# Kernel tuning notes

Measured on AMD Instinct MI355X. Metric: run time of the kernel, lower is better.

## Reference

```python
import jax, jax.numpy as jnp
import numpy as np

NMS_THR = 0.3


def pairwise_iou(b):
    # b: [N,4] in x1,y1,x2,y2
    area = (b[:, 2] - b[:, 0]) * (b[:, 3] - b[:, 1])  # [N]
    x1 = jnp.maximum(b[:, None, 0], b[None, :, 0])
    y1 = jnp.maximum(b[:, None, 1], b[None, :, 1])
    x2 = jnp.minimum(b[:, None, 2], b[None, :, 2])
    y2 = jnp.minimum(b[:, None, 3], b[None, :, 3])
    inter = jnp.clip(x2 - x1, 0.0) * jnp.clip(y2 - y1, 0.0)
    return inter / (area[:, None] + area[None, :] - inter + 1e-9)


def nms_keep(boxes, scores, valid, thr):
    # greedy NMS, fixed-shape: returns bool keep mask in original order
    N = boxes.shape[0]
    order = jnp.argsort(-jnp.where(valid, scores, -jnp.inf))
    b = boxes[order]
    v = valid[order]
    iou = pairwise_iou(b)  # [N,N]

    def step(keep, i):
        suppressed = jnp.any(keep & (iou[i] > thr))
        keep = keep.at[i].set(v[i] & jnp.logical_not(suppressed))
        return keep, None

    keep_sorted, _ = jax.lax.scan(step, jnp.zeros((N,), dtype=bool), jnp.arange(N))
    return jnp.zeros((N,), dtype=bool).at[order].set(keep_sorted)


def setup_inputs() -> dict:
    key = jax.random.key(0)
    k1, k2, k3, k4 = jax.random.split(key, 4)
    N, C, S = 6000, 81, 800
    # well-formed proposals: x1,y1 in [0, 600), w,h in [8, 200)
    xy = jax.random.uniform(k1, (N, 2), dtype=jnp.float32) * 600.0
    wh = 8.0 + jax.random.uniform(k2, (N, 2), dtype=jnp.float32) * 192.0
    proposals = jnp.concatenate([xy, xy + wh], axis=1)  # [N,4]
    reg = jax.random.normal(k3, (N, C * 4), dtype=jnp.float32)
    clss = jax.random.normal(k4, (N, C), dtype=jnp.float32) * 2.0
    stds = jnp.array([0.1, 0.1, 0.2, 0.2], dtype=jnp.float32)
    return {"proposals": proposals, "reg": reg, "clss": clss, "stds": stds, "img_size": S}


def reference(proposals, reg, clss, stds, img_size):
    N, C = clss.shape
    # anchors_bbox2offset: x1y1x2y2 -> center x,y + w,h
    w = proposals[:, 2] - proposals[:, 0]
    h = proposals[:, 3] - proposals[:, 1]
    cx = proposals[:, 0] + 0.5 * w
    cy = proposals[:, 1] + 0.5 * h
    # class selection
    probs = jax.nn.softmax(clss, axis=1)
    cls_idx = jnp.argmax(probs, axis=1)  # [N]
    score = jnp.take_along_axis(probs, cls_idx[:, None], axis=1)[:, 0]
    valid = cls_idx != 0  # non-background
    reg4 = reg.reshape(N, C, 4)
    t = jnp.take_along_axis(reg4, cls_idx[:, None, None], axis=1)[:, 0, :] * stds  # [N,4]
    # decode
    px = cx + w * t[:, 0]
    py = cy + h * t[:, 1]
    pw = w * jnp.exp(t[:, 2])
    ph = h * jnp.exp(t[:, 3])
    # offset2bbox + clip
    hi = jnp.float32(img_size - 1)
    x1 = jnp.clip(px - 0.5 * pw, 0.0, hi)
    y1 = jnp.clip(py - 0.5 * ph, 0.0, hi)
    x2 = jnp.clip(px + 0.5 * pw, 0.0, hi)
    y2 = jnp.clip(py + 0.5 * ph, 0.0, hi)
    boxes = jnp.stack((x1, y1, x2, y2), axis=1)  # [N,4]
    keep = nms_keep(jax.lax.stop_gradient(boxes), jax.lax.stop_gradient(score), valid, NMS_THR)
    m = keep.astype(boxes.dtype)
    return boxes * m[:, None], score * m, cls_idx * keep.astype(cls_idx.dtype)
```

## Files before the change

### kernel.cpp

```cpp
#include <hip/hip_runtime.h>
#include <math.h>

#define NMS_THR 0.3f
#define NACC 8

__device__ __forceinline__ float fmul(float a, float b){ return __fmul_rn(a,b); }
__device__ __forceinline__ float fadd(float a, float b){ return __fadd_rn(a,b); }
__device__ __forceinline__ float fsub(float a, float b){ return __fsub_rn(a,b); }

#define BAR_LDS() asm volatile("s_waitcnt lgkmcnt(0)\n\ts_barrier" ::: "memory")

__device__ __forceinline__ unsigned long long rdlane64(unsigned long long v, int a) {
    unsigned long long l = (unsigned int)__builtin_amdgcn_readlane((int)(unsigned int)v, a);
    unsigned long long h = (unsigned int)__builtin_amdgcn_readlane((int)(unsigned int)(v >> 32), a);
    return (h << 32) | l;
}
__device__ __forceinline__ unsigned long long rfl64(unsigned long long x){
    unsigned int lo = (unsigned int)__builtin_amdgcn_readfirstlane((int)(unsigned int)x);
    unsigned int hi = (unsigned int)__builtin_amdgcn_readfirstlane((int)(unsigned int)(x >> 32));
    return ((unsigned long long)hi << 32) | lo;
}
__device__ __forceinline__ unsigned long long waveOr64(unsigned long long v){
    for (int o = 32; o > 0; o >>= 1) v |= __shfl_xor(v, o);
    return v;
}

__global__ __launch_bounds__(256) void k_decode(
    const float* __restrict__ prop, const float* __restrict__ reg,
    const float* __restrict__ clss, const float* __restrict__ stds,
    const int* __restrict__ imgsz,
    float* __restrict__ boxes, float* __restrict__ key,
    float* __restrict__ score, int* __restrict__ cls,
    int N, int C)
{
    int wid  = threadIdx.x >> 6;
    int lane = threadIdx.x & 63;
    int n = blockIdx.x * 4 + wid;
    if (n >= N) return;
    const float* row = clss + (long)n * C;
    float ninf = -__builtin_inff();
    float x0 = (lane < C)      ? row[lane]      : ninf;
    float x1 = (lane + 64 < C) ? row[lane + 64] : ninf;
    float m = fmaxf(x0, x1);
    for (int o = 32; o > 0; o >>= 1) m = fmaxf(m, __shfl_xor(m, o));
    float e0 = (lane < C)      ? expf(x0 - m) : 0.0f;
    float e1 = (lane + 64 < C) ? expf(x1 - m) : 0.0f;
    float s = e0 + e1;
    for (int o = 32; o > 0; o >>= 1) s += __shfl_xor(s, o);
    float bv; int bi;
    if (e0 >= e1) { bv = e0; bi = lane; } else { bv = e1; bi = lane + 64; }
    for (int o = 32; o > 0; o >>= 1) {
        float ov = __shfl_xor(bv, o);
        int   oi = __shfl_xor(bi, o);
        if (ov > bv || (ov == bv && oi < bi)) { bv = ov; bi = oi; }
    }
    if (lane == 0) {
        float sc = 1.0f / s;
        int   c  = bi;
        int   valid = (c != 0);
        float p0 = prop[n*4+0], p1 = prop[n*4+1], p2 = prop[n*4+2], p3 = prop[n*4+3];
        float w  = fsub(p2, p0), h = fsub(p3, p1);
        float cx = fadd(p0, fmul(0.5f, w));
        float cy = fadd(p1, fmul(0.5f, h));
        const float* rr = reg + (long)n * C * 4 + (long)c * 4;
        float t0 = fmul(rr[0], stds[0]);
        float t1 = fmul(rr[1], stds[1]);
        float t2 = fmul(rr[2], stds[2]);
        float t3 = fmul(rr[3], stds[3]);
        float px = fadd(cx, fmul(w, t0));
        float py = fadd(cy, fmul(h, t1));
        float pw = fmul(w, expf(t2));
        float ph = fmul(h, expf(t3));
        float hi = (float)(imgsz[0] - 1);
        float bx1 = fminf(fmaxf(fsub(px, fmul(0.5f, pw)), 0.0f), hi);
        float by1 = fminf(fmaxf(fsub(py, fmul(0.5f, ph)), 0.0f), hi);
        float bx2 = fminf(fmaxf(fadd(px, fmul(0.5f, pw)), 0.0f), hi);
        float by2 = fminf(fmaxf(fadd(py, fmul(0.5f, ph)), 0.0f), hi);
        boxes[n*4+0]=bx1; boxes[n*4+1]=by1; boxes[n*4+2]=bx2; boxes[n*4+3]=by2;
        score[n] = sc;
        cls[n]   = c;
        key[n]   = valid ? sc : ninf;
    }
}

__global__ __launch_bounds__(256) void k_rank(
    const float* __restrict__ key, const float* __restrict__ boxes,
    float* __restrict__ boxesSorted, float* __restrict__ areaSorted,
    float* __restrict__ keySorted, int* __restrict__ rank,
    int* __restrict__ nValidPtr, int N)
{
    extern __shared__ float lkey[];
    __shared__ int part[256];
    int tid = threadIdx.x;
    for (int j = tid; j < N; j += 256) lkey[j] = key[j];
    __syncthreads();

    int i = blockIdx.x * 64 + (tid & 63);
    int s = tid >> 6;
    int Q = (N + 3) >> 2;
    int r_part = 0;
    if (i < N) {
        float ki = lkey[i];
        int j0 = s * Q, j1 = min(N, j0 + Q);
        for (int j = j0; j < j1; ++j) {
            float kj = lkey[j];
            r_part += (kj > ki) || (kj == ki && j < i);
        }
    }
    part[tid] = r_part;
    __syncthreads();

    if (tid < 64 && i < N) {
        int r = part[tid] + part[tid+64] + part[tid+128] + part[tid+192];
        float ki = lkey[i];
        rank[i] = r;
        float b0 = boxes[i*4+0], b1 = boxes[i*4+1], b2 = boxes[i*4+2], b3 = boxes[i*4+3];
        boxesSorted[r*4+0]=b0; boxesSorted[r*4+1]=b1; boxesSorted[r*4+2]=b2; boxesSorted[r*4+3]=b3;
        areaSorted[r] = fmul(fsub(b2,b0), fsub(b3,b1));
        keySorted[r]  = ki;
    }

    if (blockIdx.x == 0) {
        __syncthreads();
        float ninf = -__builtin_inff();
        int inv = 0;
        for (int j = tid; j < N; j += 256) inv += (lkey[j] == ninf);
        part[tid] = inv;
        __syncthreads();
        if (tid == 0) {
            int t = 0;
            for (int q = 0; q < 256; ++q) t += part[q];
            nValidPtr[0] = N - t;
        }
    }
}

__global__ __launch_bounds__(256) void k_mask(
    const float* __restrict__ bs, const float* __restrict__ areas,
    const float* __restrict__ keySorted, unsigned long long* __restrict__ mask,
    unsigned long long* __restrict__ dq,
    int N, int W, int Wpad)
{
    int wid  = threadIdx.x >> 6;
    int lane = threadIdx.x & 63;
    int i = blockIdx.x * 4 + wid;
    if (i >= N) return;
    if (keySorted[i] == -__builtin_inff()) return;
    float ax1 = bs[i*4+0], ay1 = bs[i*4+1], ax2 = bs[i*4+2], ay2 = bs[i*4+3];
    float aa  = areas[i];
    int w0 = i >> 6;
    if (lane == 0) {
        dq[i*4+0] = 0ULL; dq[i*4+1] = 0ULL; dq[i*4+2] = 0ULL; dq[i*4+3] = 0ULL;
    }
    for (int w = w0; w < W; ++w) {
        int j = w*64 + lane;
        int bit = 0;
        if (j < N && j > i) {
            float bx1 = bs[j*4+0], by1 = bs[j*4+1], bx2 = bs[j*4+2], by2 = bs[j*4+3];
            float ba  = areas[j];
            float ix1 = fmaxf(ax1,bx1), iy1 = fmaxf(ay1,by1);
            float ix2 = fminf(ax2,bx2), iy2 = fminf(ay2,by2);
            float iw = fmaxf(fsub(ix2,ix1), 0.0f);
            float ih = fmaxf(fsub(iy2,iy1), 0.0f);
            float inter = fmul(iw, ih);
            float denom = fadd(fsub(fadd(aa, ba), inter), 1e-9f);
            float iou = inter / denom;
            bit = (iou > NMS_THR) ? 1 : 0;
        }
        unsigned long long bm = __ballot(bit);
        if (lane == 0) {
            mask[(long)i*Wpad + w] = bm;
            int d = w - w0;
            if (d < 4) dq[i*4+d] = bm;
        }
    }
}

__global__ __launch_bounds__((NACC+1)*64, 1) void k_scan(
    const unsigned long long* __restrict__ mask,
    const unsigned long long* __restrict__ dq,
    const int* __restrict__ nValidPtr,
    int* __restrict__ keepSorted, int N, int W, int Wpad)
{
    __shared__ unsigned long long ldsPartA[NACC+1];
    __shared__ unsigned long long ldsPartB[NACC+1];
    __shared__ unsigned long long ldsKeepLo, ldsKeepHi;
    int tid  = threadIdx.x;
    int wid  = tid >> 6;
    int lane = tid & 63;
    for (int i = tid; i < N; i += (NACC+1)*64) keepSorted[i] = 0;
    if (tid <= NACC) { ldsPartA[tid] = 0ULL; ldsPartB[tid] = 0ULL; }
    if (tid == 0) { ldsKeepLo = 0ULL; ldsKeepHi = 0ULL; }
    __syncthreads();

    int nValid  = __builtin_amdgcn_readfirstlane(nValidPtr[0]);
    int nChunks = (nValid + 127) >> 7;

    unsigned long long A0=0,A1=0,A2=0,A3=0,B0=0,B1=0,B2=0,B3=0;
    unsigned long long sacc_prevA = 0ULL, sacc_prevB = 0ULL;
    if (wid == 0 && nChunks > 0) {
        int rA = lane, rB = 64 + lane;
        if (rA < N) {
            ulonglong2 a01 = *(const ulonglong2*)(dq + (size_t)rA*4);
            ulonglong2 a23 = *(const ulonglong2*)(dq + (size_t)rA*4 + 2);
            A0=a01.x; A1=a01.y; A2=a23.x; A3=a23.y;
        }
        if (rB < N) {
            ulonglong2 b01 = *(const ulonglong2*)(dq + (size_t)rB*4);
            ulonglong2 b23 = *(const ulonglong2*)(dq + (size_t)rB*4 + 2);
            B0=b01.x; B1=b01.y; B2=b23.x; B3=b23.y;
        }
    }
    unsigned long long accx = 0ULL, accy = 0ULL;
    bool accWave = (wid >= 1);
    int  accIdx  = wid - 1;
    bool laneok  = (2*lane + 1 < Wpad);

    for (int c = 0; c < nChunks; ++c) {
        int base = c << 7;
        if (wid == 0) {
            unsigned long long nA0=0,nA1=0,nA2=0,nA3=0,nB0=0,nB1=0,nB2=0,nB3=0;
            if (c + 1 < nChunks) {
                int rA = base + 128 + lane, rB = base + 192 + lane;
                if (rA < N) {
                    ulonglong2 a01 = *(const ulonglong2*)(dq + (size_t)rA*4);
                    ulonglong2 a23 = *(const ulonglong2*)(dq + (size_t)rA*4 + 2);
                    nA0=a01.x; nA1=a01.y; nA2=a23.x; nA3=a23.y;
                }
                if (rB < N) {
                    ulonglong2 b01 = *(const ulonglong2*)(dq + (size_t)rB*4);
                    ulonglong2 b23 = *(const ulonglong2*)(dq + (size_t)rB*4 + 2);
                    nB0=b01.x; nB1=b01.y; nB2=b23.x; nB3=b23.y;
                }
            }

            unsigned long long pA = sacc_prevA, pB = sacc_prevB;
#pragma unroll
            for (int k = 1; k <= NACC; ++k) { pA |= ldsPartA[k]; pB |= ldsPartB[k]; }
            unsigned long long incLo = rfl64(pA), incHi = rfl64(pB);
            int nv  = nValid - base;
            unsigned long long validLo = (nv >= 64) ? ~0ULL : ((1ULL << nv) - 1ULL);
            int nv2 = nv - 64;
            unsigned long long validHi = (nv2 >= 64) ? ~0ULL
                                        : (nv2 <= 0 ? 0ULL : ((1ULL << nv2) - 1ULL));
            unsigned long long candLo = validLo & ~incLo;
            unsigned long long candHi = validHi & ~incHi;
            unsigned long long keepLo = 0ULL, keepHi = 0ULL;

            unsigned long long mHiAcc = 0ULL;
            while (candLo) {
                unsigned long long t = candLo;
                int a0 = __builtin_ctzll(t); t &= t - 1;
                int a1 = t ? __builtin_ctzll(t) : a0; t &= t - 1;
                int a2 = t ? __builtin_ctzll(t) : a0; t &= t - 1;
                int a3 = t ? __builtin_ctzll(t) : a0;
                unsigned long long m0 = rdlane64(A0, a0), m1 = rdlane64(A0, a1);
                unsigned long long m2 = rdlane64(A0, a2), m3 = rdlane64(A0, a3);
                unsigned long long n0 = rdlane64(A1, a0), n1 = rdlane64(A1, a1);
                unsigned long long n2 = rdlane64(A1, a2), n3 = rdlane64(A1, a3);
                unsigned long long rem  = m0 | (1ULL << a0);
                unsigned long long kept = 1ULL << a0;
                unsigned long long hi   = n0;
                unsigned long long b;
                b = 1ULL << a1; if (!(rem & b)) { rem |= m1 | b; kept |= b; hi |= n1; }
                b = 1ULL << a2; if (!(rem & b)) { rem |= m2 | b; kept |= b; hi |= n2; }
                b = 1ULL << a3; if (!(rem & b)) { rem |= m3 | b; kept |= b; hi |= n3; }
                keepLo |= kept; mHiAcc |= hi;
                candLo &= ~rem;
            }
            candHi &= ~mHiAcc;
            while (candHi) {
                unsigned long long t = candHi;
                int a0 = __builtin_ctzll(t); t &= t - 1;
                int a1 = t ? __builtin_ctzll(t) : a0; t &= t - 1;
                int a2 = t ? __builtin_ctzll(t) : a0; t &= t - 1;
                int a3 = t ? __builtin_ctzll(t) : a0;
                unsigned long long m0 = rdlane64(B0, a0), m1 = rdlane64(B0, a1);
                unsigned long long m2 = rdlane64(B0, a2), m3 = rdlane64(B0, a3);
                unsigned long long rem  = m0 | (1ULL << a0);
                unsigned long long kept = 1ULL << a0;
                unsigned long long b;
                b = 1ULL << a1; if (!(rem & b)) { rem |= m1 | b; kept |= b; }
                b = 1ULL << a2; if (!(rem & b)) { rem |= m2 | b; kept |= b; }
                b = 1ULL << a3; if (!(rem & b)) { rem |= m3 | b; kept |= b; }
                keepHi |= kept;
                candHi &= ~rem;
            }
            {
                unsigned long long kL = (keepLo >> lane) & 1ULL;
                unsigned long long kH = (keepHi >> lane) & 1ULL;
                unsigned long long selA = (kL ? A2 : 0ULL) | (kH ? B1 : 0ULL);
                unsigned long long selB = (kL ? A3 : 0ULL) | (kH ? B2 : 0ULL);
                sacc_prevA = waveOr64(selA);
                sacc_prevB = waveOr64(selB);
            }
            if (lane == 0) { ldsKeepLo = keepLo; ldsKeepHi = keepHi; }
            if (base + lane < N)      keepSorted[base + lane]      = (int)((keepLo >> lane) & 1ULL);
            if (base + 64 + lane < N) keepSorted[base + 64 + lane] = (int)((keepHi >> lane) & 1ULL);
            A0=nA0; A1=nA1; A2=nA2; A3=nA3; B0=nB0; B1=nB1; B2=nB2; B3=nB3;
        }
        BAR_LDS();
        unsigned long long kLo = ldsKeepLo;
        unsigned long long kHi = ldsKeepHi;
        if (accWave && laneok && lane == c + 1) {
            ldsPartA[wid] = accx;
            ldsPartB[wid] = accy;
        }
        BAR_LDS();
        if (accWave && laneok) {
            unsigned int myb = (accIdx < 4)
                ? (unsigned int)((kLo >> (16*accIdx)) & 0xFFFFULL)
                : (unsigned int)((kHi >> (16*(accIdx-4))) & 0xFFFFULL);
            if (myb) {
                const unsigned long long* mb =
                    mask + (size_t)(base + 16*accIdx) * Wpad + 2*lane;
                unsigned int b = myb;
                int a0 = __builtin_ctz(b); b &= b - 1;
                int a1=-1,a2=-1,a3=-1,a4=-1,a5=-1,a6=-1,a7=-1;
                if (b) { a1 = __builtin_ctz(b); b &= b - 1; }
                if (b) { a2 = __builtin_ctz(b); b &= b - 1; }
                if (b) { a3 = __builtin_ctz(b); b &= b - 1; }
                if (b) { a4 = __builtin_ctz(b); b &= b - 1; }
                if (b) { a5 = __builtin_ctz(b); b &= b - 1; }
                if (b) { a6 = __builtin_ctz(b); b &= b - 1; }
                if (b) { a7 = __builtin_ctz(b); b &= b - 1; }
                ulonglong2 v0 = {0,0}, v1 = {0,0}, v2 = {0,0}, v3 = {0,0};
                ulonglong2 v4 = {0,0}, v5 = {0,0}, v6 = {0,0}, v7 = {0,0};
                v0 = *(const ulonglong2*)(mb + (size_t)a0 * Wpad);
                if (a1 >= 0) v1 = *(const ulonglong2*)(mb + (size_t)a1 * Wpad);
                if (a2 >= 0) v2 = *(const ulonglong2*)(mb + (size_t)a2 * Wpad);
                if (a3 >= 0) v3 = *(const ulonglong2*)(mb + (size_t)a3 * Wpad);
                if (a4 >= 0) v4 = *(const ulonglong2*)(mb + (size_t)a4 * Wpad);
                if (a5 >= 0) v5 = *(const ulonglong2*)(mb + (size_t)a5 * Wpad);
                if (a6 >= 0) v6 = *(const ulonglong2*)(mb + (size_t)a6 * Wpad);
                if (a7 >= 0) v7 = *(const ulonglong2*)(mb + (size_t)a7 * Wpad);
                accx |= ((v0.x|v1.x)|(v2.x|v3.x)) | ((v4.x|v5.x)|(v6.x|v7.x));
                accy |= ((v0.y|v1.y)|(v2.y|v3.y)) | ((v4.y|v5.y)|(v6.y|v7.y));
                while (b) {
                    int a = __builtin_ctz(b); b &= b - 1;
                    ulonglong2 v = *(const ulonglong2*)(mb + (size_t)a * Wpad);
                    accx |= v.x; accy |= v.y;
                }
            }
        }
    }
}

__global__ __launch_bounds__(256) void k_out(
    const float* __restrict__ boxes, const float* __restrict__ score,
    const int* __restrict__ cls, const int* __restrict__ rank,
    const int* __restrict__ keepSorted,
    float* __restrict__ out, int N)
{
    int n = blockIdx.x * blockDim.x + threadIdx.x;
    if (n >= N) return;
    int k = keepSorted[rank[n]];
    float m = (float)k;
    out[n*4+0] = boxes[n*4+0]*m;
    out[n*4+1] = boxes[n*4+1]*m;
    out[n*4+2] = boxes[n*4+2]*m;
    out[n*4+3] = boxes[n*4+3]*m;
    out[(long)N*4 + n] = score[n]*m;
    out[(long)N*5 + n] = (float)(cls[n] * k);
}

extern "C" void kernel_launch(void* const* d_in, const int* in_sizes, int n_in,
                              void* d_out, int out_size, void* d_ws, size_t ws_size,
                              hipStream_t stream) {
    const float* prop = (const float*)d_in[0];
    const float* reg  = (const float*)d_in[1];
    const float* clss = (const float*)d_in[2];
    const float* stds = (const float*)d_in[3];
    const int*   img  = (const int*)d_in[4];

    int N = in_sizes[0] / 4;
    int C = in_sizes[2] / N;
    int W = (N + 63) / 64;
    int Wpad = (W + 1) & ~1;

    char* ws = (char*)d_ws;
    size_t off = 0;
    float* boxes       = (float*)(ws + off); off += (size_t)N*4*sizeof(float);
    float* key         = (float*)(ws + off); off += (size_t)N*sizeof(float);
    float* score       = (float*)(ws + off); off += (size_t)N*sizeof(float);
    int*   cls         = (int*)  (ws + off); off += (size_t)N*sizeof(int);
    int*   rank        = (int*)  (ws + off); off += (size_t)N*sizeof(int);
    float* boxesSorted = (float*)(ws + off); off += (size_t)N*4*sizeof(float);
    float* areaSorted  = (float*)(ws + off); off += (size_t)N*sizeof(float);
    float* keySorted   = (float*)(ws + off); off += (size_t)N*sizeof(float);
    int*   keepSorted  = (int*)  (ws + off); off += (size_t)N*sizeof(int);
    int*   nValid      = (int*)  (ws + off); off += sizeof(int);
    off = (off + 31) & ~(size_t)31;
    unsigned long long* dq    = (unsigned long long*)(ws + off);
    off += (size_t)N * 4 * sizeof(unsigned long long);
    unsigned long long* mask  = (unsigned long long*)(ws + off);
    off += (size_t)N * Wpad * sizeof(unsigned long long);
    (void)ws_size; (void)out_size; (void)n_in;

    int rowBlocks  = (N + 3) / 4;
    int thrBlocks  = (N + 255) / 256;
    int rankBlocks = (N + 63) / 64;

    k_decode<<<rowBlocks, 256, 0, stream>>>(prop, reg, clss, stds, img,
                                            boxes, key, score, cls, N, C);
    k_rank<<<rankBlocks, 256, (size_t)N*sizeof(float), stream>>>(key, boxes,
                                            boxesSorted, areaSorted, keySorted, rank, nValid, N);
    k_mask<<<rowBlocks, 256, 0, stream>>>(boxesSorted, areaSorted, keySorted,
                                          mask, dq, N, W, Wpad);
    k_scan<<<1, (NACC+1)*64, 0, stream>>>(mask, dq, nValid, keepSorted, N, W, Wpad);
    k_out<<<thrBlocks, 256, 0, stream>>>(boxes, score, cls, rank, keepSorted,
                                         (float*)d_out, N);
}
```

Before: 185.9 us.

## Use backward-suppression bitmasks and ballot for serial in-chunk NMS resolution

The mask kernel now also emits per-row backward masks: bdiag holds the in-word earlier boxes that overlap each box, and bprev holds the overlaps against the preceding word for odd words. In the scan kernel, the sequential greedy loop within each 64-box word becomes a single ballot over the lanes' backward masks per kept box. This replaces the four-at-a-time readlane gathering of forward masks, cutting the serial dependency chain and the register traffic per step. The cost is extra IoU work and two additional small arrays written in the mask kernel, plus more ballot instructions in the loop.

Result: faster. 181.0 us (-2.7%).

```diff
diff --git a/kernel.cpp b/kernel.cpp
--- a/kernel.cpp
+++ b/kernel.cpp
@@ -10,11 +10,6 @@
 
 #define BAR_LDS() asm volatile("s_waitcnt lgkmcnt(0)\n\ts_barrier" ::: "memory")
 
-__device__ __forceinline__ unsigned long long rdlane64(unsigned long long v, int a) {
-    unsigned long long l = (unsigned int)__builtin_amdgcn_readlane((int)(unsigned int)v, a);
-    unsigned long long h = (unsigned int)__builtin_amdgcn_readlane((int)(unsigned int)(v >> 32), a);
-    return (h << 32) | l;
-}
 __device__ __forceinline__ unsigned long long rfl64(unsigned long long x){
     unsigned int lo = (unsigned int)__builtin_amdgcn_readfirstlane((int)(unsigned int)x);
     unsigned int hi = (unsigned int)__builtin_amdgcn_readfirstlane((int)(unsigned int)(x >> 32));
@@ -139,6 +134,7 @@
     const float* __restrict__ bs, const float* __restrict__ areas,
     const float* __restrict__ keySorted, unsigned long long* __restrict__ mask,
     unsigned long long* __restrict__ dq,
+    unsigned long long* __restrict__ bdiag, unsigned long long* __restrict__ bprev,
     int N, int W, int Wpad)
 {
     int wid  = threadIdx.x >> 6;
@@ -152,10 +148,10 @@
     if (lane == 0) {
         dq[i*4+0] = 0ULL; dq[i*4+1] = 0ULL; dq[i*4+2] = 0ULL; dq[i*4+3] = 0ULL;
     }
-    for (int w = w0; w < W; ++w) {
-        int j = w*64 + lane;
+    if (w0 & 1) {
+        int j = (w0 - 1) * 64 + lane;
         int bit = 0;
-        if (j < N && j > i) {
+        if (j < N) {
             float bx1 = bs[j*4+0], by1 = bs[j*4+1], bx2 = bs[j*4+2], by2 = bs[j*4+3];
             float ba  = areas[j];
             float ix1 = fmaxf(ax1,bx1), iy1 = fmaxf(ay1,by1);
@@ -168,10 +164,37 @@
             bit = (iou > NMS_THR) ? 1 : 0;
         }
         unsigned long long bm = __ballot(bit);
-        if (lane == 0) {
-            mask[(long)i*Wpad + w] = bm;
-            int d = w - w0;
-            if (d < 4) dq[i*4+d] = bm;
+        if (lane == 0) bprev[i] = bm;
+    }
+    for (int w = w0; w < W; ++w) {
+        int j = w*64 + lane;
+        int bit = 0;
+        if (j < N && j != i) {
+            float bx1 = bs[j*4+0], by1 = bs[j*4+1], bx2 = bs[j*4+2], by2 = bs[j*4+3];
+            float ba  = areas[j];
+            float ix1 = fmaxf(ax1,bx1), iy1 = fmaxf(ay1,by1);
+            float ix2 = fminf(ax2,bx2), iy2 = fminf(ay2,by2);
+            float iw = fmaxf(fsub(ix2,ix1), 0.0f);
+            float ih = fmaxf(fsub(iy2,iy1), 0.0f);
+            float inter = fmul(iw, ih);
+            float denom = fadd(fsub(fadd(aa, ba), inter), 1e-9f);
+            float iou = inter / denom;
+            bit = (iou > NMS_THR) ? 1 : 0;
+        }
+        unsigned long long fwd = __ballot(bit && (j > i));
+        if (w == w0) {
+            unsigned long long bwd = __ballot(bit && (j < i));
+            if (lane == 0) {
+                mask[(long)i*Wpad + w] = fwd;
+                dq[i*4+0] = fwd;
+                bdiag[i]  = bwd;
+            }
+        } else {
+            if (lane == 0) {
+                mask[(long)i*Wpad + w] = fwd;
+                int d = w - w0;
+                if (d < 4) dq[i*4+d] = fwd;
+            }
         }
     }
 }
@@ -179,6 +202,8 @@
 __global__ __launch_bounds__((NACC+1)*64, 1) void k_scan(
     const unsigned long long* __restrict__ mask,
     const unsigned long long* __restrict__ dq,
+    const unsigned long long* __restrict__ bdiag,
+    const unsigned long long* __restrict__ bprev,
     const int* __restrict__ nValidPtr,
     int* __restrict__ keepSorted, int N, int W, int Wpad)
 {
@@ -196,19 +221,21 @@
     int nValid  = __builtin_amdgcn_readfirstlane(nValidPtr[0]);
     int nChunks = (nValid + 127) >> 7;
 
-    unsigned long long A0=0,A1=0,A2=0,A3=0,B0=0,B1=0,B2=0,B3=0;
+    unsigned long long vA=0, vBp=0, vBd=0, A2=0, A3=0, B1=0, B2=0;
     unsigned long long sacc_prevA = 0ULL, sacc_prevB = 0ULL;
     if (wid == 0 && nChunks > 0) {
         int rA = lane, rB = 64 + lane;
         if (rA < N) {
-            ulonglong2 a01 = *(const ulonglong2*)(dq + (size_t)rA*4);
+            vA = bdiag[rA];
             ulonglong2 a23 = *(const ulonglong2*)(dq + (size_t)rA*4 + 2);
-            A0=a01.x; A1=a01.y; A2=a23.x; A3=a23.y;
+            A2 = a23.x; A3 = a23.y;
         }
         if (rB < N) {
+            vBp = bprev[rB];
+            vBd = bdiag[rB];
             ulonglong2 b01 = *(const ulonglong2*)(dq + (size_t)rB*4);
             ulonglong2 b23 = *(const ulonglong2*)(dq + (size_t)rB*4 + 2);
-            B0=b01.x; B1=b01.y; B2=b23.x; B3=b23.y;
+            B1 = b01.y; B2 = b23.x;
         }
     }
     unsigned long long accx = 0ULL, accy = 0ULL;
@@ -219,18 +246,20 @@
     for (int c = 0; c < nChunks; ++c) {
         int base = c << 7;
         if (wid == 0) {
-            unsigned long long nA0=0,nA1=0,nA2=0,nA3=0,nB0=0,nB1=0,nB2=0,nB3=0;
+            unsigned long long nvA=0, nvBp=0, nvBd=0, nA2=0, nA3=0, nB1=0, nB2=0;
             if (c + 1 < nChunks) {
                 int rA = base + 128 + lane, rB = base + 192 + lane;
                 if (rA < N) {
-                    ulonglong2 a01 = *(const ulonglong2*)(dq + (size_t)rA*4);
+                    nvA = bdiag[rA];
                     ulonglong2 a23 = *(const ulonglong2*)(dq + (size_t)rA*4 + 2);
-                    nA0=a01.x; nA1=a01.y; nA2=a23.x; nA3=a23.y;
+                    nA2 = a23.x; nA3 = a23.y;
                 }
                 if (rB < N) {
+                    nvBp = bprev[rB];
+                    nvBd = bdiag[rB];
                     ulonglong2 b01 = *(const ulonglong2*)(dq + (size_t)rB*4);
                     ulonglong2 b23 = *(const ulonglong2*)(dq + (size_t)rB*4 + 2);
-                    nB0=b01.x; nB1=b01.y; nB2=b23.x; nB3=b23.y;
+                    nB1 = b01.y; nB2 = b23.x;
                 }
             }
 
@@ -247,44 +276,20 @@
             unsigned long long candHi = validHi & ~incHi;
             unsigned long long keepLo = 0ULL, keepHi = 0ULL;
 
-            unsigned long long mHiAcc = 0ULL;
             while (candLo) {
-                unsigned long long t = candLo;
-                int a0 = __builtin_ctzll(t); t &= t - 1;
-                int a1 = t ? __builtin_ctzll(t) : a0; t &= t - 1;
-                int a2 = t ? __builtin_ctzll(t) : a0; t &= t - 1;
-                int a3 = t ? __builtin_ctzll(t) : a0;
-                unsigned long long m0 = rdlane64(A0, a0), m1 = rdlane64(A0, a1);
-                unsigned long long m2 = rdlane64(A0, a2), m3 = rdlane64(A0, a3);
-                unsigned long long n0 = rdlane64(A1, a0), n1 = rdlane64(A1, a1);
-                unsigned long long n2 = rdlane64(A1, a2), n3 = rdlane64(A1, a3);
-                unsigned long long rem  = m0 | (1ULL << a0);
-                unsigned long long kept = 1ULL << a0;
-                unsigned long long hi   = n0;
-                unsigned long long b;
-                b = 1ULL << a1; if (!(rem & b)) { rem |= m1 | b; kept |= b; hi |= n1; }
-                b = 1ULL << a2; if (!(rem & b)) { rem |= m2 | b; kept |= b; hi |= n2; }
-                b = 1ULL << a3; if (!(rem & b)) { rem |= m3 | b; kept |= b; hi |= n3; }
-                keepLo |= kept; mHiAcc |= hi;
-                candLo &= ~rem;
-            }
-            candHi &= ~mHiAcc;
+                int f = __builtin_ctzll(candLo);
+                unsigned long long sup = __ballot(((vA >> f) & 1ULL) != 0ULL);
+                unsigned long long b = 1ULL << f;
+                keepLo |= b;
+                candLo &= ~sup & ~b;
+            }
+            candHi &= ~__ballot((vBp & keepLo) != 0ULL);
             while (candHi) {
-                unsigned long long t = candHi;
-                int a0 = __builtin_ctzll(t); t &= t - 1;
-                int a1 = t ? __builtin_ctzll(t) : a0; t &= t - 1;
-                int a2 = t ? __builtin_ctzll(t) : a0; t &= t - 1;
-                int a3 = t ? __builtin_ctzll(t) : a0;
-                unsigned long long m0 = rdlane64(B0, a0), m1 = rdlane64(B0, a1);
-                unsigned long long m2 = rdlane64(B0, a2), m3 = rdlane64(B0, a3);
-                unsigned long long rem  = m0 | (1ULL << a0);
-                unsigned long long kept = 1ULL << a0;
-                unsigned long long b;
-                b = 1ULL << a1; if (!(rem & b)) { rem |= m1 | b; kept |= b; }
-                b = 1ULL << a2; if (!(rem & b)) { rem |= m2 | b; kept |= b; }
-                b = 1ULL << a3; if (!(rem & b)) { rem |= m3 | b; kept |= b; }
-                keepHi |= kept;
-                candHi &= ~rem;
+                int f = __builtin_ctzll(candHi);
+                unsigned long long sup = __ballot(((vBd >> f) & 1ULL) != 0ULL);
+                unsigned long long b = 1ULL << f;
+                keepHi |= b;
+                candHi &= ~sup & ~b;
             }
             {
                 unsigned long long kL = (keepLo >> lane) & 1ULL;
@@ -297,7 +302,7 @@
             if (lane == 0) { ldsKeepLo = keepLo; ldsKeepHi = keepHi; }
             if (base + lane < N)      keepSorted[base + lane]      = (int)((keepLo >> lane) & 1ULL);
             if (base + 64 + lane < N) keepSorted[base + 64 + lane] = (int)((keepHi >> lane) & 1ULL);
-            A0=nA0; A1=nA1; A2=nA2; A3=nA3; B0=nB0; B1=nB1; B2=nB2; B3=nB3;
+            vA=nvA; vBp=nvBp; vBd=nvBd; A2=nA2; A3=nA3; B1=nB1; B2=nB2;
         }
         BAR_LDS();
         unsigned long long kLo = ldsKeepLo;
@@ -393,6 +398,10 @@
     off = (off + 31) & ~(size_t)31;
     unsigned long long* dq    = (unsigned long long*)(ws + off);
     off += (size_t)N * 4 * sizeof(unsigned long long);
+    unsigned long long* bdiag = (unsigned long long*)(ws + off);
+    off += (size_t)N * sizeof(unsigned long long);
+    unsigned long long* bprev = (unsigned long long*)(ws + off);
+    off += (size_t)N * sizeof(unsigned long long);
     unsigned long long* mask  = (unsigned long long*)(ws + off);
     off += (size_t)N * Wpad * sizeof(unsigned long long);
     (void)ws_size; (void)out_size; (void)n_in;
@@ -406,8 +415,9 @@
     k_rank<<<rankBlocks, 256, (size_t)N*sizeof(float), stream>>>(key, boxes,
                                             boxesSorted, areaSorted, keySorted, rank, nValid, N);
     k_mask<<<rowBlocks, 256, 0, stream>>>(boxesSorted, areaSorted, keySorted,
-                                          mask, dq, N, W, Wpad);
-    k_scan<<<1, (NACC+1)*64, 0, stream>>>(mask, dq, nValid, keepSorted, N, W, Wpad);
+                                          mask, dq, bdiag, bprev, N, W, Wpad);
+    k_scan<<<1, (NACC+1)*64, 0, stream>>>(mask, dq, bdiag, bprev, nValid,
+                                          keepSorted, N, W, Wpad);
     k_out<<<thrBlocks, 256, 0, stream>>>(boxes, score, cls, rank, keepSorted,
                                          (float*)d_out, N);
 }
```
